# Performance work log

Measured on AMD Instinct MI355X. Metric: run time of the kernel, lower is better.

## Reference

```python
import jax, jax.numpy as jnp
import numpy as np

N, E, IN_DIM, H, D = 100000, 1600000, 128, 4, 32


def setup_inputs() -> dict:
    key = jax.random.key(0)
    ks = jax.random.split(key, 8)
    glorot = lambda k, shape: jax.random.uniform(
        k, shape, jnp.float32, -1.0, 1.0) * np.sqrt(6.0 / (shape[0] + shape[1]))
    return {
        "x": jax.random.normal(ks[0], (N, IN_DIM), jnp.float32),
        "row": jax.random.randint(ks[1], (E,), 0, N, jnp.int32),
        "col": jax.random.randint(ks[2], (E,), 0, N, jnp.int32),
        "W_l": glorot(ks[3], (IN_DIM, H * D)),
        "W_r": glorot(ks[4], (IN_DIM, H * D)),
        "a1w": glorot(ks[5], (IN_DIM, H)),
        "a2w": glorot(ks[6], (IN_DIM, H)),
        "bias": jnp.zeros((H * D,), jnp.float32),
    }


def reference(x, row, col, W_l, W_r, a1w, a2w, bias):
    n = x.shape[0]  # num_nodes (= graph[0].max()+1 with dense random rows)
    x_l = (x @ W_l).reshape(n, H, D)          # [N,H,D]
    x_r = x @ W_r                              # [N,H*D]
    # per-edge attention logits: a1[row] + a2[col], leaky-relu(0.2)
    attn = jax.nn.leaky_relu((x @ a1w)[row] + (x @ a2w)[col], 0.2)  # [E,H]
    # segment softmax over destination rows (numerically stable)
    m = jax.ops.segment_max(attn, row, num_segments=n)               # [N,H]
    e = jnp.exp(attn - m[row])
    s = jax.ops.segment_sum(e, row, num_segments=n)                  # [N,H]
    attn_d = e / s[row]                                              # [E,H]
    # per-head SpMM: scatter-add weighted source features to destinations
    msgs = attn_d[:, :, None] * x_l[col]                             # [E,H,D]
    out = jax.ops.segment_sum(msgs, row, num_segments=n).reshape(n, H * D)
    return out + x_r + bias
```

## Files before the change

kernel.cpp:

```cpp
#include <hip/hip_runtime.h>


typedef short bfvec8 __attribute__((ext_vector_type(8)));
typedef float f32x4  __attribute__((ext_vector_type(4)));

#define BK 128
#define CAPC 3584
#define EPB 8192
#define REC 256
#define BSTR 16

__device__ __forceinline__ unsigned short f2bf(float f) {
  union { float f; unsigned int i; } v; v.f = f;
  unsigned int r = v.i + 0x7fffu + ((v.i >> 16) & 1u);
  return (unsigned short)(r >> 16);
}

__global__ __launch_bounds__(128) void wprep_k(
    const float* __restrict__ Wl, const float* __restrict__ Wr,
    const float* __restrict__ a1w, const float* __restrict__ a2w,
    unsigned short* __restrict__ Wtg, int* __restrict__ bcur, int NBK)
{
  const int n = blockIdx.x;
  const int y = blockIdx.y;
  const int k = threadIdx.x;
  if (y == 0 && n < 8) {
    int b = n * 128 + k;
    if (b < NBK) bcur[b * BSTR] = b * CAPC;
  }
  const float* W = y ? Wr : Wl;
  const float LOG2E = 1.4426950408889634f;
  float v;
  if (n < 128)      v = W[(size_t)k * 128 + n];
  else if (y)       v = 0.f;
  else if (n < 132) v = a1w[k * 4 + (n - 128)] * LOG2E;
  else              v = a2w[k * 4 + (n - 132)] * LOG2E;
  Wtg[((size_t)y * 136 + n) * 128 + k] = f2bf(v);
}

__global__ __launch_bounds__(256) void gemm_bin_k(
    const float* __restrict__ x, const unsigned short* __restrict__ Wtg,
    const float* __restrict__ bias,
    char* __restrict__ xls, float* __restrict__ out,
    float* __restrict__ s1, float* __restrict__ s2, int N,
    const int* __restrict__ row, const int* __restrict__ col,
    int* __restrict__ bcur, unsigned int* __restrict__ binned,
    int E, int NBK, int binBlocks, int gemmBlocks)
{
  __shared__ __align__(16) char raw[32768];
  const int bid = blockIdx.x;
  const int t = threadIdx.x;
  const bool isbin = (bid % 3 == 0) && (bid / 3 < binBlocks);

  if (isbin) {
    int* h    = (int*)raw;
    int* base = (int*)(raw + 4096);
    const int sub = bid / 3;
    const int e0 = sub * EPB;
    const int e1 = min(e0 + EPB, E);

    int rloc[32];
    for (int i = t; i < NBK; i += 256) h[i] = 0;
    __syncthreads();
    #pragma unroll
    for (int k = 0; k < 32; ++k) {
      int e = e0 + t + (k << 8);
      rloc[k] = (e < e1) ? row[e] : -1;
      if (rloc[k] >= 0) atomicAdd(&h[rloc[k] >> 7], 1);
    }
    __syncthreads();
    for (int i = t; i < NBK; i += 256) {
      int c = h[i];
      base[i] = c ? atomicAdd(&bcur[i * BSTR], c) : 0;
    }
    __syncthreads();
    for (int i = t; i < NBK; i += 256) h[i] = 0;
    __syncthreads();
    #pragma unroll
    for (int k = 0; k < 32; ++k) {
      int e = e0 + t + (k << 8);
      if (e < e1) {
        int r = rloc[k];
        unsigned c = (unsigned)col[e];
        int b = r >> 7;
        int rk = atomicAdd(&h[b], 1);
        binned[base[b] + rk] = ((unsigned)(r & 127) << 17) | c;
      }
    }
    return;
  }

  unsigned short* Ws = (unsigned short*)raw;
  const int sub = bid - min(bid / 3 + 1, binBlocks);
  if (sub >= gemmBlocks) return;
  const int n0 = sub * 64;

  const int w    = t >> 6;
  const int lane = t & 63;
  const int m    = lane & 15;
  const int m7   = m & 7;
  const int quad = lane >> 4;
  const int nrow = n0 + 16 * w + m;
  const int kb   = quad * 8;

  bfvec8 afx[4];
  #pragma unroll
  for (int kc4 = 0; kc4 < 4; ++kc4) {
    f32x4 u = (f32x4){0.f, 0.f, 0.f, 0.f};
    f32x4 v = (f32x4){0.f, 0.f, 0.f, 0.f};
    if (nrow < N) {
      const float* xp = &x[(size_t)nrow * 128 + kc4 * 32 + kb];
      u = *(const f32x4*)xp;
      v = *(const f32x4*)(xp + 4);
    }
    bfvec8 a;
    a[0] = (short)f2bf(u[0]); a[1] = (short)f2bf(u[1]);
    a[2] = (short)f2bf(u[2]); a[3] = (short)f2bf(u[3]);
    a[4] = (short)f2bf(v[0]); a[5] = (short)f2bf(v[1]);
    a[6] = (short)f2bf(v[2]); a[7] = (short)f2bf(v[3]);
    afx[kc4] = a;
  }

  bfvec8 ar[4];
  {
    int arow = 128 + (m < 8 ? m : 7);
    #pragma unroll
    for (int kc4 = 0; kc4 < 4; ++kc4)
      ar[kc4] = *(const bfvec8*)&Wtg[(size_t)arow * 128 + kc4 * 32 + kb];
  }

  #pragma unroll
  for (int y = 0; y < 2; ++y) {
    const unsigned short* Wt = Wtg + (size_t)y * 136 * 128;
    if (y) __syncthreads();
    for (int i = t; i < 2048; i += 256) {
      int nr = i >> 4, g = i & 15;
      int gs = (g ^ (nr & 7)) << 3;
      *(uint4*)&Ws[nr * 128 + gs] = *(const uint4*)&Wt[(size_t)nr * 128 + (g << 3)];
    }
    __syncthreads();

    f32x4 acc[9];
    #pragma unroll
    for (int i = 0; i < 9; ++i) acc[i] = (f32x4){0.f, 0.f, 0.f, 0.f};

    #pragma unroll
    for (int kc4 = 0; kc4 < 4; ++kc4) {
      #pragma unroll
      for (int nt = 0; nt < 8; ++nt) {
        int g = kc4 * 4 + quad;
        bfvec8 bfr = *(const bfvec8*)&Ws[(nt * 16 + m) * 128 + ((g ^ m7) << 3)];
        acc[nt] = __builtin_amdgcn_mfma_f32_16x16x32_bf16(bfr, afx[kc4], acc[nt], 0, 0, 0);
      }
      if (y == 0)
        acc[8] = __builtin_amdgcn_mfma_f32_16x16x32_bf16(ar[kc4], afx[kc4], acc[8], 0, 0, 0);
    }

    if (nrow < N) {
      if (y) {
        #pragma unroll
        for (int nt = 0; nt < 8; ++nt) {
          int c = nt * 16 + quad * 4;
          float4 b4 = *(const float4*)&bias[c];
          float4 v = make_float4(acc[nt][0] + b4.x, acc[nt][1] + b4.y,
                                 acc[nt][2] + b4.z, acc[nt][3] + b4.w);
          *(float4*)&out[(size_t)nrow * 128 + c] = v;
        }
      } else {
        #pragma unroll
        for (int nt = 0; nt < 8; ++nt) {
          int c = nt * 16 + quad * 4;
          unsigned lo = (unsigned)f2bf(acc[nt][0]) | ((unsigned)f2bf(acc[nt][1]) << 16);
          unsigned hi = (unsigned)f2bf(acc[nt][2]) | ((unsigned)f2bf(acc[nt][3]) << 16);
          *(uint2*)(xls + ((size_t)nrow << 8) + 2 * c) = make_uint2(lo, hi);
        }
        if (quad == 0) *(f32x4*)&s1[nrow * 4] = acc[8];
        else if (quad == 1) *(f32x4*)&s2[nrow * 4] = acc[8];
      }
    }
  }
}

__global__ __launch_bounds__(256) void csr_k(const unsigned int* __restrict__ binned,
    const int* __restrict__ bcur, int* __restrict__ offs, int* __restrict__ deg,
    unsigned int* __restrict__ colsort, int N)
{
  __shared__ unsigned ecache[CAPC];
  __shared__ int h[BK];
  __shared__ int sh[BK];
  const int t = threadIdx.x;
  const int b = blockIdx.x;
  const int lo = b * BK;
  const int e0 = b * CAPC;
  const int e1 = bcur[b * BSTR];

  if (t < BK) h[t] = 0;
  __syncthreads();
  for (int i = e0 + t; i < e1; i += 256) {
    unsigned p = binned[i];
    ecache[i - e0] = p;
    atomicAdd(&h[p >> 17], 1);
  }
  __syncthreads();

  int v = 0;
  if (t < BK) { v = h[t]; sh[t] = v; }
  __syncthreads();
  for (int off = 1; off < BK; off <<= 1) {
    int tv = (t < BK && t >= off) ? sh[t - off] : 0;
    __syncthreads();
    if (t < BK) sh[t] += tv;
    __syncthreads();
  }
  if (t < BK) {
    int ex = sh[t] - v;
    int node = lo + t;
    if (node < N) { offs[node] = e0 + ex; deg[node] = v; }
    h[t] = ex;
  }
  __syncthreads();
  const int cnt = e1 - e0;
  for (int i = t; i < cnt; i += 256) {
    unsigned p = ecache[i];
    int rlo = p >> 17;
    unsigned c = p & 0x1FFFFu;
    int pos = atomicAdd(&h[rlo], 1);
    colsort[e0 + pos] = c << 8;
  }
}

__global__ __launch_bounds__(256) void agg_k(const int* __restrict__ offs,
    const int* __restrict__ deg, const unsigned int* __restrict__ colsort,
    const float* __restrict__ s1, const float* __restrict__ s2,
    const char* __restrict__ xls, float* __restrict__ out, int N)
{
  const int lane = threadIdx.x & 63;
  const int n = blockIdx.x * 4 + (threadIdx.x >> 6);
  if (n >= N) return;
  const int e0 = offs[n], e1 = e0 + deg[n];
  const int h  = lane >> 4;
  const int hp = lane & 3;
  const int jj = (lane >> 2) & 7;
  const float s1c = s1[n * 4 + hp];
  const unsigned lane4 = (unsigned)(lane << 2);
  const unsigned hp4   = (unsigned)(hp << 2);
  const char* s2b = (const char*)s2;

  float acc0 = 0.f, acc1 = 0.f, wsum = 0.f;
  int i0 = e0;
  for (; i0 + 8 <= e1; i0 += 8) {
    unsigned csl = colsort[i0 + jj];
    float z2 = *(const float*)(s2b + ((csl >> 4) + hp4));
    float z = s1c + z2;
    z = fmaxf(z, 0.2f * z);
    float wv = exp2f(z);

    unsigned cs[8];
    #pragma unroll
    for (int j = 0; j < 8; ++j) cs[j] = colsort[i0 + j];
    unsigned pv[8];
    #pragma unroll
    for (int j = 0; j < 8; ++j)
      pv[j] = *(const unsigned*)(xls + (cs[j] + lane4));

    #pragma unroll
    for (int j = 0; j < 8; ++j) {
      float wj = __shfl(wv, (j << 2) | h);
      wsum += wj;
      union { unsigned u; float f; } lo, hi;
      lo.u = pv[j] << 16;
      hi.u = pv[j] & 0xffff0000u;
      acc0 += wj * lo.f;
      acc1 += wj * hi.f;
    }
  }
  if (i0 < e1) {
    const int rem = e1 - i0;
    unsigned csl = colsort[i0 + (jj < rem ? jj : rem - 1)];
    float z2 = *(const float*)(s2b + ((csl >> 4) + hp4));
    float z = s1c + z2;
    z = fmaxf(z, 0.2f * z);
    float wv = (jj < rem) ? exp2f(z) : 0.f;

    unsigned cs[8];
    #pragma unroll
    for (int j = 0; j < 8; ++j) cs[j] = colsort[i0 + (j < rem ? j : rem - 1)];
    unsigned pv[8];
    #pragma unroll
    for (int j = 0; j < 8; ++j)
      pv[j] = *(const unsigned*)(xls + (cs[j] + lane4));

    #pragma unroll
    for (int j = 0; j < 8; ++j) {
      float wj = __shfl(wv, (j << 2) | h);
      wsum += wj;
      union { unsigned u; float f; } lo, hi;
      lo.u = pv[j] << 16;
      hi.u = pv[j] & 0xffff0000u;
      acc0 += wj * lo.f;
      acc1 += wj * hi.f;
    }
  }

  float inv = (wsum > 0.f) ? (1.0f / wsum) : 0.f;
  const size_t o = (size_t)n * 128 + 2 * lane;
  float2 xr = *(const float2*)&out[o];
  float2 res; res.x = acc0 * inv + xr.x; res.y = acc1 * inv + xr.y;
  *(float2*)&out[o] = res;
}

extern "C" void kernel_launch(void* const* d_in, const int* in_sizes, int n_in,
                              void* d_out, int out_size, void* d_ws, size_t ws_size,
                              hipStream_t stream) {
  const float* x    = (const float*)d_in[0];
  const int*   row  = (const int*)d_in[1];
  const int*   col  = (const int*)d_in[2];
  const float* Wl   = (const float*)d_in[3];
  const float* Wr   = (const float*)d_in[4];
  const float* a1w  = (const float*)d_in[5];
  const float* a2w  = (const float*)d_in[6];
  const float* bias = (const float*)d_in[7];
  float* out = (float*)d_out;
  const int N = in_sizes[0] / 128;
  const int E = in_sizes[1];
  (void)n_in; (void)out_size; (void)ws_size;

  const int NBK = (N + BK - 1) / BK;

  char* ws = (char*)d_ws;
  size_t off = 0;
  auto carve = [&](size_t bytes) { void* p = ws + off; off += (bytes + 255) & ~(size_t)255; return p; };
  char* xls            = (char*)carve((size_t)N * REC);
  float* s1            = (float*)carve((size_t)N * 4 * 4);
  float* s2            = (float*)carve((size_t)N * 4 * 4);
  int* offs            = (int*)carve((size_t)N * 4);
  int* deg             = (int*)carve((size_t)N * 4);
  unsigned int* colsort= (unsigned int*)carve((size_t)NBK * CAPC * 4);
  unsigned int* binned = (unsigned int*)carve((size_t)NBK * CAPC * 4);
  int* bcur            = (int*)carve((size_t)NBK * BSTR * 4);
  unsigned short* Wtg  = (unsigned short*)carve((size_t)2 * 136 * 128 * 2);

  const int gemmBlocks = (N + 63) / 64;
  const int binBlocks  = (E + EPB - 1) / EPB;
  const int T = gemmBlocks + binBlocks;

  wprep_k   <<<dim3(136, 2), 128, 0, stream>>>(Wl, Wr, a1w, a2w, Wtg, bcur, NBK);
  gemm_bin_k<<<T, 256, 0, stream>>>(x, Wtg, bias, xls, out, s1, s2, N,
                                    row, col, bcur, binned, E, NBK,
                                    binBlocks, gemmBlocks);
  csr_k     <<<NBK, 256, 0, stream>>>(binned, bcur, offs, deg, colsort, N);
  agg_k     <<<(N + 3) / 4, 256, 0, stream>>>(offs, deg, colsort, s1, s2, xls, out, N);
}
```

Measured before the change: 256.8 us.

## Fuse CSR build and aggregation into one kernel with LDS-resident sorted columns

Merges the CSR construction kernel and the aggregation kernel into a single 1024-thread block per 128-node bucket. Column indices are counting-sorted into shared memory, and 16 waves then each aggregate 8 nodes straight from that LDS copy. This removes the global colsort, offs and deg arrays along with one kernel launch. The cost is fewer, larger blocks (about 782) carrying roughly 28KB of LDS each, which lowers occupancy and can leave load imbalance within a block.

```diff
diff --git a/kernel.cpp b/kernel.cpp
--- a/kernel.cpp
+++ b/kernel.cpp
@@ -181,30 +181,32 @@
   }
 }
 
-__global__ __launch_bounds__(256) void csr_k(const unsigned int* __restrict__ binned,
-    const int* __restrict__ bcur, int* __restrict__ offs, int* __restrict__ deg,
-    unsigned int* __restrict__ colsort, int N)
+__global__ __launch_bounds__(1024) void csragg_k(
+    const unsigned int* __restrict__ binned, const int* __restrict__ bcur,
+    const float* __restrict__ s1, const float* __restrict__ s2,
+    const char* __restrict__ xls, float* __restrict__ out, int N)
 {
   __shared__ unsigned ecache[CAPC];
+  __shared__ unsigned scol[CAPC];
   __shared__ int h[BK];
   __shared__ int sh[BK];
+  __shared__ int dg[BK];
   const int t = threadIdx.x;
   const int b = blockIdx.x;
   const int lo = b * BK;
-  const int e0 = b * CAPC;
-  const int e1 = bcur[b * BSTR];
+  const int e0g = b * CAPC;
+  const int e1g = bcur[b * BSTR];
 
   if (t < BK) h[t] = 0;
   __syncthreads();
-  for (int i = e0 + t; i < e1; i += 256) {
+  for (int i = e0g + t; i < e1g; i += 1024) {
     unsigned p = binned[i];
-    ecache[i - e0] = p;
+    ecache[i - e0g] = p;
     atomicAdd(&h[p >> 17], 1);
   }
   __syncthreads();
-
   int v = 0;
-  if (t < BK) { v = h[t]; sh[t] = v; }
+  if (t < BK) { v = h[t]; sh[t] = v; dg[t] = v; }
   __syncthreads();
   for (int off = 1; off < BK; off <<= 1) {
     int tv = (t < BK && t >= off) ? sh[t - off] : 0;
@@ -212,101 +214,95 @@
     if (t < BK) sh[t] += tv;
     __syncthreads();
   }
-  if (t < BK) {
-    int ex = sh[t] - v;
-    int node = lo + t;
-    if (node < N) { offs[node] = e0 + ex; deg[node] = v; }
-    h[t] = ex;
-  }
-  __syncthreads();
-  const int cnt = e1 - e0;
-  for (int i = t; i < cnt; i += 256) {
+  if (t < BK) h[t] = sh[t] - v;
+  __syncthreads();
+  const int cnt = e1g - e0g;
+  for (int i = t; i < cnt; i += 1024) {
     unsigned p = ecache[i];
-    int rlo = p >> 17;
-    unsigned c = p & 0x1FFFFu;
-    int pos = atomicAdd(&h[rlo], 1);
-    colsort[e0 + pos] = c << 8;
-  }
-}
-
-__global__ __launch_bounds__(256) void agg_k(const int* __restrict__ offs,
-    const int* __restrict__ deg, const unsigned int* __restrict__ colsort,
-    const float* __restrict__ s1, const float* __restrict__ s2,
-    const char* __restrict__ xls, float* __restrict__ out, int N)
-{
-  const int lane = threadIdx.x & 63;
-  const int n = blockIdx.x * 4 + (threadIdx.x >> 6);
-  if (n >= N) return;
-  const int e0 = offs[n], e1 = e0 + deg[n];
-  const int h  = lane >> 4;
-  const int hp = lane & 3;
-  const int jj = (lane >> 2) & 7;
-  const float s1c = s1[n * 4 + hp];
+    int pos = atomicAdd(&h[p >> 17], 1);
+    scol[pos] = (p & 0x1FFFFu) << 8;
+  }
+  __syncthreads();
+
+  const int wvi  = t >> 6;
+  const int lane = t & 63;
+  const int hd   = lane >> 4;
+  const int hp   = lane & 3;
+  const int jj   = (lane >> 2) & 7;
   const unsigned lane4 = (unsigned)(lane << 2);
   const unsigned hp4   = (unsigned)(hp << 2);
   const char* s2b = (const char*)s2;
 
-  float acc0 = 0.f, acc1 = 0.f, wsum = 0.f;
-  int i0 = e0;
-  for (; i0 + 8 <= e1; i0 += 8) {
-    unsigned csl = colsort[i0 + jj];
-    float z2 = *(const float*)(s2b + ((csl >> 4) + hp4));
-    float z = s1c + z2;
-    z = fmaxf(z, 0.2f * z);
-    float wv = exp2f(z);
-
-    unsigned cs[8];
-    #pragma unroll
-    for (int j = 0; j < 8; ++j) cs[j] = colsort[i0 + j];
-    unsigned pv[8];
-    #pragma unroll
-    for (int j = 0; j < 8; ++j)
-      pv[j] = *(const unsigned*)(xls + (cs[j] + lane4));
-
-    #pragma unroll
-    for (int j = 0; j < 8; ++j) {
-      float wj = __shfl(wv, (j << 2) | h);
-      wsum += wj;
-      union { unsigned u; float f; } lo, hi;
-      lo.u = pv[j] << 16;
-      hi.u = pv[j] & 0xffff0000u;
-      acc0 += wj * lo.f;
-      acc1 += wj * hi.f;
-    }
-  }
-  if (i0 < e1) {
-    const int rem = e1 - i0;
-    unsigned csl = colsort[i0 + (jj < rem ? jj : rem - 1)];
-    float z2 = *(const float*)(s2b + ((csl >> 4) + hp4));
-    float z = s1c + z2;
-    z = fmaxf(z, 0.2f * z);
-    float wv = (jj < rem) ? exp2f(z) : 0.f;
-
-    unsigned cs[8];
-    #pragma unroll
-    for (int j = 0; j < 8; ++j) cs[j] = colsort[i0 + (j < rem ? j : rem - 1)];
-    unsigned pv[8];
-    #pragma unroll
-    for (int j = 0; j < 8; ++j)
-      pv[j] = *(const unsigned*)(xls + (cs[j] + lane4));
-
-    #pragma unroll
-    for (int j = 0; j < 8; ++j) {
-      float wj = __shfl(wv, (j << 2) | h);
-      wsum += wj;
-      union { unsigned u; float f; } lo, hi;
-      lo.u = pv[j] << 16;
-      hi.u = pv[j] & 0xffff0000u;
-      acc0 += wj * lo.f;
-      acc1 += wj * hi.f;
-    }
-  }
-
-  float inv = (wsum > 0.f) ? (1.0f / wsum) : 0.f;
-  const size_t o = (size_t)n * 128 + 2 * lane;
-  float2 xr = *(const float2*)&out[o];
-  float2 res; res.x = acc0 * inv + xr.x; res.y = acc1 * inv + xr.y;
-  *(float2*)&out[o] = res;
+  for (int q = 0; q < 8; ++q) {
+    const int nl = wvi * 8 + q;
+    const int node = lo + nl;
+    if (node >= N) break;
+    const int eS = h[nl] - dg[nl];
+    const int eE = h[nl];
+    const float s1c = s1[node * 4 + hp];
+
+    float acc0 = 0.f, acc1 = 0.f, wsum = 0.f;
+    int i0 = eS;
+    for (; i0 + 8 <= eE; i0 += 8) {
+      unsigned csl = scol[i0 + jj];
+      float z2 = *(const float*)(s2b + ((csl >> 4) + hp4));
+      float z = s1c + z2;
+      z = fmaxf(z, 0.2f * z);
+      float wv = exp2f(z);
+
+      unsigned cs[8];
+      #pragma unroll
+      for (int j = 0; j < 8; ++j) cs[j] = scol[i0 + j];
+      unsigned pv[8];
+      #pragma unroll
+      for (int j = 0; j < 8; ++j)
+        pv[j] = *(const unsigned*)(xls + (cs[j] + lane4));
+
+      #pragma unroll
+      for (int j = 0; j < 8; ++j) {
+        float wj = __shfl(wv, (j << 2) | hd);
+        wsum += wj;
+        union { unsigned u; float f; } lof, hif;
+        lof.u = pv[j] << 16;
+        hif.u = pv[j] & 0xffff0000u;
+        acc0 += wj * lof.f;
+        acc1 += wj * hif.f;
+      }
+    }
+    if (i0 < eE) {
+      const int rem = eE - i0;
+      unsigned csl = scol[i0 + (jj < rem ? jj : rem - 1)];
+      float z2 = *(const float*)(s2b + ((csl >> 4) + hp4));
+      float z = s1c + z2;
+      z = fmaxf(z, 0.2f * z);
+      float wv = (jj < rem) ? exp2f(z) : 0.f;
+
+      unsigned cs[8];
+      #pragma unroll
+      for (int j = 0; j < 8; ++j) cs[j] = scol[i0 + (j < rem ? j : rem - 1)];
+      unsigned pv[8];
+      #pragma unroll
+      for (int j = 0; j < 8; ++j)
+        pv[j] = *(const unsigned*)(xls + (cs[j] + lane4));
+
+      #pragma unroll
+      for (int j = 0; j < 8; ++j) {
+        float wj = __shfl(wv, (j << 2) | hd);
+        wsum += wj;
+        union { unsigned u; float f; } lof, hif;
+        lof.u = pv[j] << 16;
+        hif.u = pv[j] & 0xffff0000u;
+        acc0 += wj * lof.f;
+        acc1 += wj * hif.f;
+      }
+    }
+
+    float inv = (wsum > 0.f) ? (1.0f / wsum) : 0.f;
+    const size_t o = (size_t)node * 128 + 2 * lane;
+    float2 xr = *(const float2*)&out[o];
+    float2 res; res.x = acc0 * inv + xr.x; res.y = acc1 * inv + xr.y;
+    *(float2*)&out[o] = res;
+  }
 }
 
 extern "C" void kernel_launch(void* const* d_in, const int* in_sizes, int n_in,
@@ -333,9 +329,6 @@
   char* xls            = (char*)carve((size_t)N * REC);
   float* s1            = (float*)carve((size_t)N * 4 * 4);
   float* s2            = (float*)carve((size_t)N * 4 * 4);
-  int* offs            = (int*)carve((size_t)N * 4);
-  int* deg             = (int*)carve((size_t)N * 4);
-  unsigned int* colsort= (unsigned int*)carve((size_t)NBK * CAPC * 4);
   unsigned int* binned = (unsigned int*)carve((size_t)NBK * CAPC * 4);
   int* bcur            = (int*)carve((size_t)NBK * BSTR * 4);
   unsigned short* Wtg  = (unsigned short*)carve((size_t)2 * 136 * 128 * 2);
@@ -348,6 +341,5 @@
   gemm_bin_k<<<T, 256, 0, stream>>>(x, Wtg, bias, xls, out, s1, s2, N,
                                     row, col, bcur, binned, E, NBK,
                                     binBlocks, gemmBlocks);
-  csr_k     <<<NBK, 256, 0, stream>>>(binned, bcur, offs, deg, colsort, N);
-  agg_k     <<<(N + 3) / 4, 256, 0, stream>>>(offs, deg, colsort, s1, s2, xls, out, N);
-}
+  csragg_k  <<<NBK, 1024, 0, stream>>>(binned, bcur, s1, s2, xls, out, N);
+}
```

After: 256.0 us. About the same (-0.3%).
